# Optimization experiments

Hardware: AMD Instinct MI355X
Metric: run time of the kernel (lower is better)

## Reference

```python
import jax, jax.numpy as jnp
import numpy as np

N, E = 4096, 131072
IN_DIM, HID, OUT_DIM = 128, 64, 128
H1 = 4                       # gat1 heads
D_MODEL = HID * H1           # 256
NHEAD = 4
D_FF = 2048


def setup_inputs() -> dict:
    key = jax.random.key(0)
    ks = jax.random.split(key, 16)
    def w(k, shape, scale=0.05):
        return jax.random.normal(k, shape, dtype=jnp.float32) * scale
    return {
        "x": jax.random.normal(ks[0], (N, IN_DIM), dtype=jnp.float32),
        "edge_index": jax.random.randint(ks[1], (2, E), 0, N, dtype=jnp.int32),
        "gat1_w": w(ks[2], (H1 * HID, IN_DIM)),
        "gat1_asrc": w(ks[3], (H1, HID)),
        "gat1_adst": w(ks[4], (H1, HID)),
        "gat1_b": jnp.zeros((H1 * HID,), jnp.float32),
        "in_proj_w": w(ks[5], (3 * D_MODEL, D_MODEL)),
        "in_proj_b": jnp.zeros((3 * D_MODEL,), jnp.float32),
        "out_proj_w": w(ks[6], (D_MODEL, D_MODEL)),
        "out_proj_b": jnp.zeros((D_MODEL,), jnp.float32),
        "lin1_w": w(ks[7], (D_FF, D_MODEL)),
        "lin1_b": jnp.zeros((D_FF,), jnp.float32),
        "lin2_w": w(ks[8], (D_MODEL, D_FF)),
        "lin2_b": jnp.zeros((D_MODEL,), jnp.float32),
        "ln1_g": jnp.ones((D_MODEL,), jnp.float32),
        "ln1_b": jnp.zeros((D_MODEL,), jnp.float32),
        "ln2_g": jnp.ones((D_MODEL,), jnp.float32),
        "ln2_b": jnp.zeros((D_MODEL,), jnp.float32),
        "gat2_w": w(ks[9], (OUT_DIM, D_MODEL)),
        "gat2_asrc": w(ks[10], (1, OUT_DIM)),
        "gat2_adst": w(ks[11], (1, OUT_DIM)),
        "gat2_b": jnp.zeros((OUT_DIM,), jnp.float32),
    }


def _add_self_loops(ei, n):
    loops = jnp.arange(n, dtype=ei.dtype)
    return jnp.concatenate([ei, jnp.stack([loops, loops])], axis=1)


def _segment_softmax(logits, seg, n):
    # numerically stable softmax over edges grouped by destination node
    m = jax.ops.segment_max(logits, seg, num_segments=n)
    m = jnp.where(jnp.isfinite(m), m, 0.0)
    e = jnp.exp(logits - m[seg])
    s = jax.ops.segment_sum(e, seg, num_segments=n)
    return e / (s[seg] + 1e-16)


def _gat(x, ei, W, asrc, adst, b, heads, out_ch):
    n = x.shape[0]
    h = (x @ W.T).reshape(n, heads, out_ch)          # [N,H,C]
    al_s = jnp.einsum('nhc,hc->nh', h, asrc)
    al_d = jnp.einsum('nhc,hc->nh', h, adst)
    src, dst = ei[0], ei[1]
    logits = jax.nn.leaky_relu(al_s[src] + al_d[dst], 0.2)   # [E,H]
    alpha = _segment_softmax(logits, dst, n)
    out = jax.ops.segment_sum(h[src] * alpha[:, :, None], dst, num_segments=n)
    return out.reshape(n, heads * out_ch) + b


def _ln(x, g, b):
    mu = x.mean(-1, keepdims=True)
    v = x.var(-1, keepdims=True)
    return (x - mu) / jnp.sqrt(v + 1e-5) * g + b


def _forward(x, edge_index, gat1_w, gat1_asrc, gat1_adst, gat1_b,
             in_proj_w, in_proj_b, out_proj_w, out_proj_b,
             lin1_w, lin1_b, lin2_w, lin2_b, ln1_g, ln1_b, ln2_g, ln2_b,
             gat2_w, gat2_asrc, gat2_adst, gat2_b):
    n = x.shape[0]
    ei = _add_self_loops(edge_index, n)
    h = jax.nn.elu(_gat(x, ei, gat1_w, gat1_asrc, gat1_adst, gat1_b, H1, HID))  # [N, 256]
    # TransformerEncoderLayer (post-norm, relu, no dropout in eval)
    hd = D_MODEL // NHEAD
    qkv = h @ in_proj_w.T + in_proj_b
    q, k, v = jnp.split(qkv, 3, axis=-1)
    q = q.reshape(n, NHEAD, hd)
    k = k.reshape(n, NHEAD, hd)
    v = v.reshape(n, NHEAD, hd)
    scores = jnp.einsum('qhd,khd->hqk', q, k) / jnp.sqrt(jnp.float32(hd))
    attn = jax.nn.softmax(scores, axis=-1)
    o = jnp.einsum('hqk,khd->qhd', attn, v).reshape(n, D_MODEL)
    o = o @ out_proj_w.T + out_proj_b
    h = _ln(h + o, ln1_g, ln1_b)
    ff = jax.nn.relu(h @ lin1_w.T + lin1_b) @ lin2_w.T + lin2_b
    h = _ln(h + ff, ln2_g, ln2_b)
    return _gat(h, ei, gat2_w, gat2_asrc, gat2_adst, gat2_b, 1, OUT_DIM)


def reference(x, edge_index, gat1_w, gat1_asrc, gat1_adst, gat1_b,
              in_proj_w, in_proj_b, out_proj_w, out_proj_b,
              lin1_w, lin1_b, lin2_w, lin2_b, ln1_g, ln1_b, ln2_g, ln2_b,
              gat2_w, gat2_asrc, gat2_adst, gat2_b):
    return _forward(x, edge_index, gat1_w, gat1_asrc, gat1_adst, gat1_b,
                    in_proj_w, in_proj_b, out_proj_w, out_proj_b,
                    lin1_w, lin1_b, lin2_w, lin2_b, ln1_g, ln1_b, ln2_g, ln2_b,
                    gat2_w, gat2_asrc, gat2_adst, gat2_b)
```

## Files before the change

kernel.cpp:

```cpp
#include <hip/hip_runtime.h>
#include <hip/hip_bf16.h>
#include <math.h>

#define NN 4096
#define NE 131072
#define EE (NE + NN)

typedef unsigned short u16;
typedef short s8v __attribute__((ext_vector_type(8)));
typedef float f4v __attribute__((ext_vector_type(4)));
typedef float f16v __attribute__((ext_vector_type(16)));

__device__ inline u16 f2b(float f) {
  __hip_bfloat16 h = __float2bfloat16(f);
  return __builtin_bit_cast(u16, h);
}
__device__ inline float b2f(u16 v) {
  unsigned int u = ((unsigned int)v) << 16;
  return __builtin_bit_cast(float, u);
}

__global__ void k_count(const int* __restrict__ ei, int* __restrict__ deg) {
  int e = blockIdx.x * 256 + threadIdx.x;
  if (e >= EE) return;
  int dst = (e < NE) ? ei[NE + e] : (e - NE);
  atomicAdd(&deg[dst], 1);
}

__global__ __launch_bounds__(1024) void k_scan(const int* __restrict__ deg, int* __restrict__ rowptr) {
  __shared__ int lds[1024];
  int t = threadIdx.x;
  int v0 = deg[t*4+0], v1 = deg[t*4+1], v2 = deg[t*4+2], v3 = deg[t*4+3];
  int s1 = v0+v1, s2 = s1+v2, s3 = s2+v3;
  lds[t] = s3;
  __syncthreads();
  for (int off = 1; off < 1024; off <<= 1) {
    int add = (t >= off) ? lds[t-off] : 0;
    __syncthreads();
    lds[t] += add;
    __syncthreads();
  }
  int base = lds[t] - s3;
  rowptr[t*4+1] = base + v0;
  rowptr[t*4+2] = base + s1;
  rowptr[t*4+3] = base + s2;
  rowptr[t*4+4] = base + s3;
  if (t == 0) rowptr[0] = 0;
}

__global__ void k_scatter(const int* __restrict__ ei, const int* __restrict__ rowptr,
                          int* __restrict__ cursor, int* __restrict__ csr_src) {
  int e = blockIdx.x * 256 + threadIdx.x;
  if (e >= EE) return;
  int src, dst;
  if (e < NE) { src = ei[e]; dst = ei[NE + e]; }
  else { src = e - NE; dst = src; }
  int pos = rowptr[dst] + atomicAdd(&cursor[dst], 1);
  csr_src[pos] = src;
}

__global__ __launch_bounds__(256) void k_f2b_all(
    const float* a0, u16* b0, int e0, const float* a1, u16* b1, int e1,
    const float* a2, u16* b2, int e2, const float* a3, u16* b3, int e3,
    const float* a4, u16* b4, int e4, const float* a5, u16* b5, int e5,
    const float* a6, u16* b6, int e6)
{
  int i = blockIdx.x * 256 + threadIdx.x;
  const float* s; u16* d; int base;
  if      (i < e0) { s=a0; d=b0; base=0;  }
  else if (i < e1) { s=a1; d=b1; base=e0; }
  else if (i < e2) { s=a2; d=b2; base=e1; }
  else if (i < e3) { s=a3; d=b3; base=e2; }
  else if (i < e4) { s=a4; d=b4; base=e3; }
  else if (i < e5) { s=a5; d=b5; base=e4; }
  else if (i < e6) { s=a6; d=b6; base=e5; }
  else return;
  int j = i - base;
  float4 v = ((const float4*)s)[j];
  u16 r[4] = {f2b(v.x), f2b(v.y), f2b(v.z), f2b(v.w)};
  *(uint2*)(d + (size_t)j*4) = *(uint2*)r;
}

template<int HEADS, int C>
__global__ __launch_bounds__(256) void k_alogits(
    const u16* __restrict__ featb, const float* __restrict__ asrc,
    const float* __restrict__ adst, float* __restrict__ als, float* __restrict__ ald)
{
  constexpr int F = HEADS * C;
  int n = blockIdx.x, t = threadIdx.x;
  __shared__ float red[F];
  float f = b2f(featb[(size_t)n*F + t]);
  int hh = t / C, cc = t % C;
  red[t] = f * asrc[t];
  __syncthreads();
  for (int off = C/2; off > 0; off >>= 1) {
    float add = (cc < off) ? red[t + off] : 0.f;
    __syncthreads();
    if (cc < off) red[t] += add;
    __syncthreads();
  }
  if (cc == 0) als[(size_t)n*HEADS + hh] = red[t];
  __syncthreads();
  red[t] = f * adst[t];
  __syncthreads();
  for (int off = C/2; off > 0; off >>= 1) {
    float add = (cc < off) ? red[t + off] : 0.f;
    __syncthreads();
    if (cc < off) red[t] += add;
    __syncthreads();
  }
  if (cc == 0) ald[(size_t)n*HEADS + hh] = red[t];
}

template<int HEADS, int C, bool DO_ELU, bool WB>
__global__ __launch_bounds__(256) void k_gat_agg(
    const u16* __restrict__ featb, const float* __restrict__ als,
    const float* __restrict__ ald, const float* __restrict__ bias,
    const int* __restrict__ rowptr, const int* __restrict__ csr_src,
    float* __restrict__ out, u16* __restrict__ outb)
{
  constexpr int F = HEADS * C;
  int n = blockIdx.x, t = threadIdx.x;
  __shared__ float m_sh[HEADS], s_sh[HEADS];
  int start = rowptr[n];
  int deg = rowptr[n+1] - start;
  int lane = t & 63, wv = t >> 6;
  for (int hh = wv; hh < HEADS; hh += F/64) {
    float adl = ald[(size_t)n*HEADS + hh];
    float mx = -INFINITY;
    for (int i = lane; i < deg; i += 64) {
      int s = csr_src[start + i];
      float lg = als[(size_t)s*HEADS + hh] + adl;
      lg = (lg > 0.f) ? lg : 0.2f * lg;
      mx = fmaxf(mx, lg);
    }
    #pragma unroll
    for (int off = 32; off; off >>= 1) mx = fmaxf(mx, __shfl_xor(mx, off));
    float sm = 0.f;
    for (int i = lane; i < deg; i += 64) {
      int s = csr_src[start + i];
      float lg = als[(size_t)s*HEADS + hh] + adl;
      lg = (lg > 0.f) ? lg : 0.2f * lg;
      sm += expf(lg - mx);
    }
    #pragma unroll
    for (int off = 32; off; off >>= 1) sm += __shfl_xor(sm, off);
    if (lane == 0) { m_sh[hh] = mx; s_sh[hh] = sm; }
  }
  __syncthreads();
  int hh = t / C;
  float adl = ald[(size_t)n*HEADS + hh];
  float mh = m_sh[hh];
  float acc0 = 0.f, acc1 = 0.f;
  int i = 0;
  for (; i + 1 < deg; i += 2) {
    int s0 = csr_src[start + i];
    int s1 = csr_src[start + i + 1];
    float lg0 = als[(size_t)s0*HEADS + hh] + adl;
    float lg1 = als[(size_t)s1*HEADS + hh] + adl;
    lg0 = (lg0 > 0.f) ? lg0 : 0.2f * lg0;
    lg1 = (lg1 > 0.f) ? lg1 : 0.2f * lg1;
    float p0 = expf(lg0 - mh);
    float p1 = expf(lg1 - mh);
    acc0 += p0 * b2f(featb[(size_t)s0*F + t]);
    acc1 += p1 * b2f(featb[(size_t)s1*F + t]);
  }
  if (i < deg) {
    int s0 = csr_src[start + i];
    float lg0 = als[(size_t)s0*HEADS + hh] + adl;
    lg0 = (lg0 > 0.f) ? lg0 : 0.2f * lg0;
    acc0 += expf(lg0 - mh) * b2f(featb[(size_t)s0*F + t]);
  }
  float o = (acc0 + acc1) / (s_sh[hh] + 1e-16f) + bias[t];
  if (DO_ELU) o = (o > 0.f) ? o : (expf(o) - 1.f);
  out[(size_t)n*F + t] = o;
  if (WB) outb[(size_t)n*F + t] = f2b(o);
}

template<int MODE>
__global__ __launch_bounds__(256) void k_gemm_mfma(
    const u16* __restrict__ A, const u16* __restrict__ B,
    const float* __restrict__ bias, float* __restrict__ Cf, u16* __restrict__ Cb,
    u16* __restrict__ Qb, u16* __restrict__ Kb, u16* __restrict__ Vt,
    int M, int N, int K)
{
  __shared__ u16 Al[64*64];
  __shared__ u16 Bl[64*64];
  char* Ab = (char*)Al;
  char* Bb = (char*)Bl;
  const int t = threadIdx.x;
  const int lane = t & 63;
  const int lr = lane & 15, lk = lane >> 4;
  const int wid = t >> 6;
  const int wm = wid & 1, wn = wid >> 1;
  const int m0 = blockIdx.y * 64, n0 = blockIdx.x * 64;

  f4v acc[2][2];
  #pragma unroll
  for (int mi = 0; mi < 2; ++mi)
    #pragma unroll
    for (int ni = 0; ni < 2; ++ni)
      acc[mi][ni] = f4v{0.f, 0.f, 0.f, 0.f};

  for (int k0 = 0; k0 < K; k0 += 64) {
    #pragma unroll
    for (int i = 0; i < 2; ++i) {
      int idx = t + i*256;
      int row = idx >> 3, ch = idx & 7;
      s8v av = *(const s8v*)(A + (size_t)(m0 + row)*K + k0 + ch*8);
      *(s8v*)(Ab + row*128 + ((ch*16) ^ ((row & 7) << 4))) = av;
      s8v bv = *(const s8v*)(B + (size_t)(n0 + row)*K + k0 + ch*8);
      *(s8v*)(Bb + row*128 + ((ch*16) ^ ((row & 7) << 4))) = bv;
    }
    __syncthreads();
    #pragma unroll
    for (int ks = 0; ks < 2; ++ks) {
      s8v af[2], bfr[2];
      #pragma unroll
      for (int mi = 0; mi < 2; ++mi) {
        int row = wm*32 + mi*16 + lr;
        int ch = ks*4 + lk;
        af[mi] = *(const s8v*)(Ab + row*128 + ((ch*16) ^ ((row & 7) << 4)));
      }
      #pragma unroll
      for (int ni = 0; ni < 2; ++ni) {
        int row = wn*32 + ni*16 + lr;
        int ch = ks*4 + lk;
        bfr[ni] = *(const s8v*)(Bb + row*128 + ((ch*16) ^ ((row & 7) << 4)));
      }
      #pragma unroll
      for (int mi = 0; mi < 2; ++mi)
        #pragma unroll
        for (int ni = 0; ni < 2; ++ni)
          acc[mi][ni] = __builtin_amdgcn_mfma_f32_16x16x32_bf16(af[mi], bfr[ni], acc[mi][ni], 0, 0, 0);
    }
    __syncthreads();
  }
  #pragma unroll
  for (int ni = 0; ni < 2; ++ni) {
    int col = n0 + wn*32 + ni*16 + lr;
    float bc = bias ? bias[col] : 0.f;
    #pragma unroll
    for (int mi = 0; mi < 2; ++mi) {
      int row0 = m0 + wm*32 + mi*16 + lk*4;
      float v[4];
      #pragma unroll
      for (int r = 0; r < 4; ++r) {
        v[r] = acc[mi][ni][r] + bc;
        if (MODE == 1) v[r] = fmaxf(v[r], 0.f);
      }
      if (MODE == 0) {
        #pragma unroll
        for (int r = 0; r < 4; ++r) Cf[(size_t)(row0 + r)*N + col] = v[r];
      } else if (MODE == 1 || MODE == 2) {
        #pragma unroll
        for (int r = 0; r < 4; ++r) Cb[(size_t)(row0 + r)*N + col] = f2b(v[r]);
      } else {
        if (col < 512) {
          int head = (col >> 6) & 3;
          int d = col & 63;
          u16* dst = ((col < 256) ? Qb : Kb) + (size_t)head*262144 + d;
          #pragma unroll
          for (int r = 0; r < 4; ++r) dst[(size_t)(row0 + r)*64] = f2b(v[r]);
        } else {
          int cc = col - 512;
          int head = cc >> 6;
          int d = cc & 63;
          int quad = row0 & 12;
          int qs = (quad == 4) ? 8 : ((quad == 8) ? 4 : quad);
          size_t nphys = (size_t)((row0 & ~15) | qs);
          u16 o4[4];
          #pragma unroll
          for (int r = 0; r < 4; ++r) o4[r] = f2b(v[r]);
          *(uint2*)(Vt + (size_t)head*262144 + (size_t)d*4096 + nphys) = *(uint2*)o4;
        }
      }
    }
  }
}

__global__ __launch_bounds__(256) void k_gemm_sk(
    const u16* __restrict__ A, const u16* __restrict__ B,
    float* __restrict__ Po, int M, int N, int K)
{
  __shared__ u16 Al[64*64];
  __shared__ u16 Bl[64*64];
  char* Ab = (char*)Al;
  char* Bb = (char*)Bl;
  const int t = threadIdx.x;
  const int lane = t & 63;
  const int lr = lane & 15, lk = lane >> 4;
  const int wid = t >> 6;
  const int wm = wid & 1, wn = wid >> 1;
  const int m0 = blockIdx.y * 64, n0 = blockIdx.x * 64;
  const int z = blockIdx.z;
  const int ksl = K >> 2;

  f4v acc[2][2];
  #pragma unroll
  for (int mi = 0; mi < 2; ++mi)
    #pragma unroll
    for (int ni = 0; ni < 2; ++ni)
      acc[mi][ni] = f4v{0.f, 0.f, 0.f, 0.f};

  for (int k0 = z*ksl; k0 < (z+1)*ksl; k0 += 64) {
    #pragma unroll
    for (int i = 0; i < 2; ++i) {
      int idx = t + i*256;
      int row = idx >> 3, ch = idx & 7;
      s8v av = *(const s8v*)(A + (size_t)(m0 + row)*K + k0 + ch*8);
      *(s8v*)(Ab + row*128 + ((ch*16) ^ ((row & 7) << 4))) = av;
      s8v bv = *(const s8v*)(B + (size_t)(n0 + row)*K + k0 + ch*8);
      *(s8v*)(Bb + row*128 + ((ch*16) ^ ((row & 7) << 4))) = bv;
    }
    __syncthreads();
    #pragma unroll
    for (int ks = 0; ks < 2; ++ks) {
      s8v af[2], bfr[2];
      #pragma unroll
      for (int mi = 0; mi < 2; ++mi) {
        int row = wm*32 + mi*16 + lr;
        int ch = ks*4 + lk;
        af[mi] = *(const s8v*)(Ab + row*128 + ((ch*16) ^ ((row & 7) << 4)));
      }
      #pragma unroll
      for (int ni = 0; ni < 2; ++ni) {
        int row = wn*32 + ni*16 + lr;
        int ch = ks*4 + lk;
        bfr[ni] = *(const s8v*)(Bb + row*128 + ((ch*16) ^ ((row & 7) << 4)));
      }
      #pragma unroll
      for (int mi = 0; mi < 2; ++mi)
        #pragma unroll
        for (int ni = 0; ni < 2; ++ni)
          acc[mi][ni] = __builtin_amdgcn_mfma_f32_16x16x32_bf16(af[mi], bfr[ni], acc[mi][ni], 0, 0, 0);
    }
    __syncthreads();
  }
  float* Pz = Po + (size_t)z * M * N;
  #pragma unroll
  for (int ni = 0; ni < 2; ++ni) {
    int col = n0 + wn*32 + ni*16 + lr;
    #pragma unroll
    for (int mi = 0; mi < 2; ++mi) {
      int row0 = m0 + wm*32 + mi*16 + lk*4;
      #pragma unroll
      for (int r = 0; r < 4; ++r)
        Pz[(size_t)(row0 + r)*N + col] = acc[mi][ni][r];
    }
  }
}

template<bool WB>
__global__ __launch_bounds__(256) void k_ln(
    const float* __restrict__ a, const float* __restrict__ res,
    const float* __restrict__ g, const float* __restrict__ bb,
    float* __restrict__ out, u16* __restrict__ outb)
{
  int n = blockIdx.x, t = threadIdx.x;
  __shared__ float part[4];
  float v = a[(size_t)n*256 + t] + res[(size_t)n*256 + t];
  float s = v;
  #pragma unroll
  for (int off = 32; off; off >>= 1) s += __shfl_xor(s, off);
  if ((t & 63) == 0) part[t >> 6] = s;
  __syncthreads();
  float mean = (part[0] + part[1] + part[2] + part[3]) * (1.f/256.f);
  __syncthreads();
  float d = v - mean;
  float s2 = d * d;
  #pragma unroll
  for (int off = 32; off; off >>= 1) s2 += __shfl_xor(s2, off);
  if ((t & 63) == 0) part[t >> 6] = s2;
  __syncthreads();
  float var = (part[0] + part[1] + part[2] + part[3]) * (1.f/256.f);
  float rstd = rsqrtf(var + 1e-5f);
  float o = d * rstd * g[t] + bb[t];
  out[(size_t)n*256 + t] = o;
  if (WB) outb[(size_t)n*256 + t] = f2b(o);
}

template<bool WB>
__global__ __launch_bounds__(256) void k_ln_sk(
    const float* __restrict__ Po, const float* __restrict__ bias,
    const float* __restrict__ res, const float* __restrict__ g,
    const float* __restrict__ bb, float* __restrict__ out, u16* __restrict__ outb)
{
  int n = blockIdx.x, t = threadIdx.x;
  __shared__ float part[4];
  const size_t MN = (size_t)NN * 256;
  size_t idx = (size_t)n*256 + t;
  float v = Po[idx] + Po[MN + idx] + Po[2*MN + idx] + Po[3*MN + idx]
          + bias[t] + res[idx];
  float s = v;
  #pragma unroll
  for (int off = 32; off; off >>= 1) s += __shfl_xor(s, off);
  if ((t & 63) == 0) part[t >> 6] = s;
  __syncthreads();
  float mean = (part[0] + part[1] + part[2] + part[3]) * (1.f/256.f);
  __syncthreads();
  float d = v - mean;
  float s2 = d * d;
  #pragma unroll
  for (int off = 32; off; off >>= 1) s2 += __shfl_xor(s2, off);
  if ((t & 63) == 0) part[t >> 6] = s2;
  __syncthreads();
  float var = (part[0] + part[1] + part[2] + part[3]) * (1.f/256.f);
  float rstd = rsqrtf(var + 1e-5f);
  float o = d * rstd * g[t] + bb[t];
  out[idx] = o;
  if (WB) outb[idx] = f2b(o);
}

__global__ __launch_bounds__(512) void k_attn2(
    const u16* __restrict__ Qb, const u16* __restrict__ Kb,
    const u16* __restrict__ Vt, u16* __restrict__ attno_b)
{
  const int strip = blockIdx.x;
  const int head  = blockIdx.y;
  const int q0 = strip * 32;
  const int t = threadIdx.x;
  const int s = t >> 6;
  const int l = t & 63;
  const int lq = l & 31;
  const int lh = l >> 5;

  __shared__ float lds_O[4][32][68];
  __shared__ float lds_m[4][32];
  __shared__ float lds_l[4][32];

  const u16* Qh = Qb + (size_t)head * (4096*64);
  const u16* Kh = Kb + (size_t)head * (4096*64);
  const u16* Vh = Vt + (size_t)head * (64*4096);

  s8v qf[4];
#pragma unroll
  for (int dc = 0; dc < 4; ++dc)
    qf[dc] = *(const s8v*)(Qh + (size_t)(q0 + lq)*64 + dc*16 + lh*8);

  f16v accO[2];
#pragma unroll
  for (int dm = 0; dm < 2; ++dm)
#pragma unroll
    for (int i = 0; i < 16; ++i) accO[dm][i] = 0.f;

  float mrow = -INFINITY, lrow = 0.f;
  const float CE = 0.18033688011112042f;

  const int kt0 = s * 512;
  for (int kt = kt0; kt < kt0 + 512; kt += 64) {
    f16v st[2];
#pragma unroll
    for (int c = 0; c < 2; ++c)
#pragma unroll
      for (int i = 0; i < 16; ++i) st[c][i] = 0.f;
    __builtin_amdgcn_s_setprio(1);
#pragma unroll
    for (int dc = 0; dc < 4; ++dc) {
      s8v kf0 = *(const s8v*)(Kh + (size_t)(kt + lq)*64 + dc*16 + lh*8);
      s8v kf1 = *(const s8v*)(Kh + (size_t)(kt + 32 + lq)*64 + dc*16 + lh*8);
      st[0] = __builtin_amdgcn_mfma_f32_32x32x16_bf16(kf0, qf[dc], st[0], 0, 0, 0);
      st[1] = __builtin_amdgcn_mfma_f32_32x32x16_bf16(kf1, qf[dc], st[1], 0, 0, 0);
    }
    __builtin_amdgcn_s_setprio(0);
    float tm[16];
#pragma unroll
    for (int i = 0; i < 8; ++i) tm[i]   = fmaxf(st[0][2*i], st[0][2*i+1]);
#pragma unroll
    for (int i = 0; i < 8; ++i) tm[8+i] = fmaxf(st[1][2*i], st[1][2*i+1]);
#pragma unroll
    for (int w = 8; w >= 1; w >>= 1)
#pragma unroll
      for (int i = 0; i < 8; ++i) if (i < w) tm[i] = fmaxf(tm[i], tm[i+w]);
    float mx = fmaxf(tm[0], __shfl_xor(tm[0], 32));
    float mn;
    if (__all(mx - mrow <= 66.0f)) {
      mn = mrow;
    } else {
      mn = fmaxf(mrow, mx);
      float sc = exp2f((mrow - mn) * CE);
      mrow = mn;
      lrow *= sc;
#pragma unroll
      for (int dm = 0; dm < 2; ++dm)
#pragma unroll
        for (int i = 0; i < 16; ++i) accO[dm][i] *= sc;
    }
    float ts[16];
#pragma unroll
    for (int c = 0; c < 2; ++c)
#pragma unroll
      for (int i = 0; i < 16; ++i)
        st[c][i] = exp2f((st[c][i] - mn) * CE);
#pragma unroll
    for (int i = 0; i < 8; ++i) ts[i]   = st[0][2*i] + st[0][2*i+1];
#pragma unroll
    for (int i = 0; i < 8; ++i) ts[8+i] = st[1][2*i] + st[1][2*i+1];
#pragma unroll
    for (int w = 8; w >= 1; w >>= 1)
#pragma unroll
      for (int i = 0; i < 8; ++i) if (i < w) ts[i] += ts[i+w];
    float ps = ts[0] + __shfl_xor(ts[0], 32);
    lrow += ps;

#pragma unroll
    for (int c = 0; c < 2; ++c) {
#pragma unroll
      for (int kc = 0; kc < 2; ++kc) {
        union { s8v v; unsigned int w[4]; } pb;
#pragma unroll
        for (int wd = 0; wd < 4; ++wd) {
          u16 lo16 = f2b(st[c][kc*8 + wd*2]);
          u16 hi16 = f2b(st[c][kc*8 + wd*2 + 1]);
          pb.w[wd] = (unsigned int)lo16 | ((unsigned int)hi16 << 16);
        }
        __builtin_amdgcn_s_setprio(1);
#pragma unroll
        for (int dm = 0; dm < 2; ++dm) {
          s8v vf = *(const s8v*)(Vh + (size_t)(dm*32 + lq)*4096 + kt + c*32 + kc*16 + lh*8);
          accO[dm] = __builtin_amdgcn_mfma_f32_32x32x16_bf16(vf, pb.v, accO[dm], 0, 0, 0);
        }
        __builtin_amdgcn_s_setprio(0);
      }
    }
  }

#pragma unroll
  for (int lev = 0; lev < 3; ++lev) {
    const int step = 1 << lev;
    __syncthreads();
    if ((s & (2*step - 1)) == step) {
      int slot = (s - step) >> (lev + 1);
      if (l < 32) { lds_m[slot][lq] = mrow; lds_l[slot][lq] = lrow; }
#pragma unroll
      for (int dm = 0; dm < 2; ++dm)
#pragma unroll
        for (int g = 0; g < 4; ++g) {
          f4v v;
#pragma unroll
          for (int rr = 0; rr < 4; ++rr) v[rr] = accO[dm][g*4 + rr];
          *(f4v*)&lds_O[slot][lq][dm*32 + lh*4 + g*8] = v;
        }
    }
    __syncthreads();
    if ((s & (2*step - 1)) == 0) {
      int slot = s >> (lev + 1);
      float mp = lds_m[slot][lq], lp = lds_l[slot][lq];
      float M = fmaxf(mrow, mp);
      float w0 = exp2f((mrow - M) * CE);
      float w1 = exp2f((mp - M) * CE);
      lrow = lrow * w0 + lp * w1;
      mrow = M;
#pragma unroll
      for (int dm = 0; dm < 2; ++dm)
#pragma unroll
        for (int g = 0; g < 4; ++g) {
          f4v vp = *(const f4v*)&lds_O[slot][lq][dm*32 + lh*4 + g*8];
#pragma unroll
          for (int rr = 0; rr < 4; ++rr)
            accO[dm][g*4 + rr] = accO[dm][g*4 + rr] * w0 + vp[rr] * w1;
        }
    }
  }

  if (s == 0) {
    float inv = 1.f / lrow;
#pragma unroll
    for (int dm = 0; dm < 2; ++dm)
#pragma unroll
      for (int g = 0; g < 4; ++g) {
        u16 o4[4];
#pragma unroll
        for (int rr = 0; rr < 4; ++rr) o4[rr] = f2b(accO[dm][g*4 + rr] * inv);
        *(uint2*)(attno_b + (size_t)(q0 + lq)*256 + head*64 + dm*32 + lh*4 + g*8) = *(uint2*)o4;
      }
  }
}

extern "C" void kernel_launch(void* const* d_in, const int* in_sizes, int n_in,
                              void* d_out, int out_size, void* d_ws, size_t ws_size,
                              hipStream_t stream)
{
  const float* x       = (const float*)d_in[0];
  const int*   ei      = (const int*)d_in[1];
  const float* gat1_w  = (const float*)d_in[2];
  const float* gat1_as = (const float*)d_in[3];
  const float* gat1_ad = (const float*)d_in[4];
  const float* gat1_b  = (const float*)d_in[5];
  const float* inp_w   = (const float*)d_in[6];
  const float* inp_b   = (const float*)d_in[7];
  const float* outp_w  = (const float*)d_in[8];
  const float* outp_b  = (const float*)d_in[9];
  const float* lin1_w  = (const float*)d_in[10];
  const float* lin1_b  = (const float*)d_in[11];
  const float* lin2_w  = (const float*)d_in[12];
  const float* lin2_b  = (const float*)d_in[13];
  const float* ln1_g   = (const float*)d_in[14];
  const float* ln1_bb  = (const float*)d_in[15];
  const float* ln2_g   = (const float*)d_in[16];
  const float* ln2_bb  = (const float*)d_in[17];
  const float* gat2_w  = (const float*)d_in[18];
  const float* gat2_as = (const float*)d_in[19];
  const float* gat2_ad = (const float*)d_in[20];
  const float* gat2_b  = (const float*)d_in[21];
  float* out = (float*)d_out;
  (void)in_sizes; (void)n_in; (void)out_size; (void)ws_size;

  char* ws = (char*)d_ws;
  size_t off = 0;
  auto nxt = [&](size_t bytes) { size_t r = off; off += (bytes + 255) & ~(size_t)255; return r; };
  int* deg      = (int*)(ws + nxt((size_t)NN*4));
  int* cursor   = (int*)(ws + nxt((size_t)NN*4));
  int* rowptr   = (int*)(ws + nxt((size_t)(NN+1)*4));
  int* csr_src  = (int*)(ws + nxt((size_t)EE*4));
  float* al1s   = (float*)(ws + nxt((size_t)NN*4*4));
  float* al1d   = (float*)(ws + nxt((size_t)NN*4*4));
  float* hgat1  = (float*)(ws + nxt((size_t)NN*256*4));
  float* tmp256 = (float*)(ws + nxt((size_t)NN*256*4));
  float* hln1   = (float*)(ws + nxt((size_t)NN*256*4));
  float* hln2   = (float*)(ws + nxt((size_t)NN*256*4));
  float* Po     = (float*)(ws + nxt((size_t)4*NN*256*4));
  float* al2s   = (float*)(ws + nxt((size_t)NN*4));
  float* al2d   = (float*)(ws + nxt((size_t)NN*4));
  u16* x_b      = (u16*)(ws + nxt((size_t)NN*128*2));
  u16* feat1_b  = (u16*)(ws + nxt((size_t)NN*256*2));
  u16* feat2_b  = (u16*)(ws + nxt((size_t)NN*128*2));
  u16* hgat1_b  = (u16*)(ws + nxt((size_t)NN*256*2));
  u16* attno_b  = (u16*)(ws + nxt((size_t)NN*256*2));
  u16* hln1_b   = (u16*)(ws + nxt((size_t)NN*256*2));
  u16* hln2_b   = (u16*)(ws + nxt((size_t)NN*256*2));
  u16* ff1_b    = (u16*)(ws + nxt((size_t)NN*2048*2));
  u16* Qb       = (u16*)(ws + nxt((size_t)4*4096*64*2));
  u16* Kb       = (u16*)(ws + nxt((size_t)4*4096*64*2));
  u16* Vt       = (u16*)(ws + nxt((size_t)4*4096*64*2));
  u16* inp_w_b  = (u16*)(ws + nxt((size_t)768*256*2));
  u16* outp_w_b = (u16*)(ws + nxt((size_t)256*256*2));
  u16* lin1_w_b = (u16*)(ws + nxt((size_t)2048*256*2));
  u16* lin2_w_b = (u16*)(ws + nxt((size_t)256*2048*2));
  u16* gat1_w_b = (u16*)(ws + nxt((size_t)256*128*2));
  u16* gat2_w_b = (u16*)(ws + nxt((size_t)128*256*2));

  hipMemsetAsync(deg, 0, (size_t)NN*4, stream);
  hipMemsetAsync(cursor, 0, (size_t)NN*4, stream);
  k_count<<<(EE+255)/256, 256, 0, stream>>>(ei, deg);
  k_scan<<<1, 1024, 0, stream>>>(deg, rowptr);
  k_scatter<<<(EE+255)/256, 256, 0, stream>>>(ei, rowptr, cursor, csr_src);

  k_f2b_all<<<1856, 256, 0, stream>>>(
      inp_w,  inp_w_b,  49152,
      outp_w, outp_w_b, 65536,
      lin1_w, lin1_w_b, 196608,
      lin2_w, lin2_w_b, 327680,
      gat1_w, gat1_w_b, 335872,
      gat2_w, gat2_w_b, 344064,
      x,      x_b,      475136);

  k_gemm_mfma<2><<<dim3(4, 64), 256, 0, stream>>>(x_b, gat1_w_b, nullptr, nullptr, feat1_b, nullptr, nullptr, nullptr, NN, 256, 128);
  k_alogits<4,64><<<NN, 256, 0, stream>>>(feat1_b, gat1_as, gat1_ad, al1s, al1d);
  k_gat_agg<4,64,true,true><<<NN, 256, 0, stream>>>(feat1_b, al1s, al1d, gat1_b, rowptr, csr_src, hgat1, hgat1_b);

  k_gemm_mfma<3><<<dim3(12, 64), 256, 0, stream>>>(hgat1_b, inp_w_b, inp_b, nullptr, nullptr, Qb, Kb, Vt, NN, 768, 256);
  k_attn2<<<dim3(128, 4), 512, 0, stream>>>(Qb, Kb, Vt, attno_b);
  k_gemm_mfma<0><<<dim3(4, 64), 256, 0, stream>>>(attno_b, outp_w_b, outp_b, tmp256, nullptr, nullptr, nullptr, nullptr, NN, 256, 256);
  k_ln<true><<<NN, 256, 0, stream>>>(tmp256, hgat1, ln1_g, ln1_bb, hln1, hln1_b);
  k_gemm_mfma<1><<<dim3(32, 64), 256, 0, stream>>>(hln1_b, lin1_w_b, lin1_b, nullptr, ff1_b, nullptr, nullptr, nullptr, NN, 2048, 256);
  k_gemm_sk<<<dim3(4, 64, 4), 256, 0, stream>>>(ff1_b, lin2_w_b, Po, NN, 256, 2048);
  k_ln_sk<true><<<NN, 256, 0, stream>>>(Po, lin2_b, hln1, ln2_g, ln2_bb, hln2, hln2_b);

  k_gemm_mfma<2><<<dim3(2, 64), 256, 0, stream>>>(hln2_b, gat2_w_b, nullptr, nullptr, feat2_b, nullptr, nullptr, nullptr, NN, 128, 256);
  k_alogits<1,128><<<NN, 128, 0, stream>>>(feat2_b, gat2_as, gat2_ad, al2s, al2d);
  k_gat_agg<1,128,false,false><<<NN, 128, 0, stream>>>(feat2_b, al2s, al2d, gat2_b, rowptr, csr_src, out, nullptr);
}
```

Baseline: 307.6 us.

## Split attention over keys, retile FFN GEMMs, cache GAT alphas, shuffle reductions

```diff
diff --git a/kernel.cpp b/kernel.cpp
--- a/kernel.cpp
+++ b/kernel.cpp
@@ -88,28 +88,29 @@
 {
   constexpr int F = HEADS * C;
   int n = blockIdx.x, t = threadIdx.x;
-  __shared__ float red[F];
   float f = b2f(featb[(size_t)n*F + t]);
-  int hh = t / C, cc = t % C;
-  red[t] = f * asrc[t];
-  __syncthreads();
-  for (int off = C/2; off > 0; off >>= 1) {
-    float add = (cc < off) ? red[t + off] : 0.f;
-    __syncthreads();
-    if (cc < off) red[t] += add;
-    __syncthreads();
-  }
-  if (cc == 0) als[(size_t)n*HEADS + hh] = red[t];
-  __syncthreads();
-  red[t] = f * adst[t];
-  __syncthreads();
-  for (int off = C/2; off > 0; off >>= 1) {
-    float add = (cc < off) ? red[t + off] : 0.f;
-    __syncthreads();
-    if (cc < off) red[t] += add;
-    __syncthreads();
-  }
-  if (cc == 0) ald[(size_t)n*HEADS + hh] = red[t];
+  float ps = f * asrc[t];
+  float pd = f * adst[t];
+  #pragma unroll
+  for (int off = 32; off; off >>= 1) {
+    ps += __shfl_xor(ps, off);
+    pd += __shfl_xor(pd, off);
+  }
+  if constexpr (C == 64) {
+    if ((t & 63) == 0) {
+      int hh = t >> 6;
+      als[(size_t)n*HEADS + hh] = ps;
+      ald[(size_t)n*HEADS + hh] = pd;
+    }
+  } else {
+    __shared__ float sh[2][2];
+    if ((t & 63) == 0) { sh[t>>6][0] = ps; sh[t>>6][1] = pd; }
+    __syncthreads();
+    if (t == 0) {
+      als[n] = sh[0][0] + sh[1][0];
+      ald[n] = sh[0][1] + sh[1][1];
+    }
+  }
 }
 
 template<int HEADS, int C, bool DO_ELU, bool WB>
@@ -122,6 +123,8 @@
   constexpr int F = HEADS * C;
   int n = blockIdx.x, t = threadIdx.x;
   __shared__ float m_sh[HEADS], s_sh[HEADS];
+  __shared__ float alpha_sh[HEADS][64];
+  __shared__ int src_sh[64];
   int start = rowptr[n];
   int deg = rowptr[n+1] - start;
   int lane = t & 63, wv = t >> 6;
@@ -149,27 +152,29 @@
   }
   __syncthreads();
   int hh = t / C;
-  float adl = ald[(size_t)n*HEADS + hh];
-  float mh = m_sh[hh];
+  int hh2 = t >> 6;
+  int ia = t & 63;
   float acc0 = 0.f, acc1 = 0.f;
-  int i = 0;
-  for (; i + 1 < deg; i += 2) {
-    int s0 = csr_src[start + i];
-    int s1 = csr_src[start + i + 1];
-    float lg0 = als[(size_t)s0*HEADS + hh] + adl;
-    float lg1 = als[(size_t)s1*HEADS + hh] + adl;
-    lg0 = (lg0 > 0.f) ? lg0 : 0.2f * lg0;
-    lg1 = (lg1 > 0.f) ? lg1 : 0.2f * lg1;
-    float p0 = expf(lg0 - mh);
-    float p1 = expf(lg1 - mh);
-    acc0 += p0 * b2f(featb[(size_t)s0*F + t]);
-    acc1 += p1 * b2f(featb[(size_t)s1*F + t]);
-  }
-  if (i < deg) {
-    int s0 = csr_src[start + i];
-    float lg0 = als[(size_t)s0*HEADS + hh] + adl;
-    lg0 = (lg0 > 0.f) ? lg0 : 0.2f * lg0;
-    acc0 += expf(lg0 - mh) * b2f(featb[(size_t)s0*F + t]);
+  for (int c0 = 0; c0 < deg; c0 += 64) {
+    int cn = min(64, deg - c0);
+    if (hh2 < HEADS && ia < cn) {
+      int s = csr_src[start + c0 + ia];
+      if (hh2 == 0) src_sh[ia] = s;
+      float lg = als[(size_t)s*HEADS + hh2] + ald[(size_t)n*HEADS + hh2];
+      lg = (lg > 0.f) ? lg : 0.2f * lg;
+      alpha_sh[hh2][ia] = expf(lg - m_sh[hh2]);
+    }
+    __syncthreads();
+    int i = 0;
+    for (; i + 1 < cn; i += 2) {
+      int s0 = src_sh[i], s1 = src_sh[i+1];
+      float a0 = alpha_sh[hh][i], a1 = alpha_sh[hh][i+1];
+      acc0 += a0 * b2f(featb[(size_t)s0*F + t]);
+      acc1 += a1 * b2f(featb[(size_t)s1*F + t]);
+    }
+    if (i < cn)
+      acc0 += alpha_sh[hh][i] * b2f(featb[(size_t)src_sh[i]*F + t]);
+    __syncthreads();
   }
   float o = (acc0 + acc1) / (s_sh[hh] + 1e-16f) + bias[t];
   if (DO_ELU) o = (o > 0.f) ? o : (expf(o) - 1.f);
@@ -245,14 +250,11 @@
       int row0 = m0 + wm*32 + mi*16 + lk*4;
       float v[4];
       #pragma unroll
-      for (int r = 0; r < 4; ++r) {
-        v[r] = acc[mi][ni][r] + bc;
-        if (MODE == 1) v[r] = fmaxf(v[r], 0.f);
-      }
+      for (int r = 0; r < 4; ++r) v[r] = acc[mi][ni][r] + bc;
       if (MODE == 0) {
         #pragma unroll
         for (int r = 0; r < 4; ++r) Cf[(size_t)(row0 + r)*N + col] = v[r];
-      } else if (MODE == 1 || MODE == 2) {
+      } else if (MODE == 2) {
         #pragma unroll
         for (int r = 0; r < 4; ++r) Cb[(size_t)(row0 + r)*N + col] = f2b(v[r]);
       } else {
@@ -279,74 +281,87 @@
   }
 }
 
-__global__ __launch_bounds__(256) void k_gemm_sk(
+template<int MODE>
+__global__ __launch_bounds__(256) void k_gemm2(
     const u16* __restrict__ A, const u16* __restrict__ B,
-    float* __restrict__ Po, int M, int N, int K)
-{
-  __shared__ u16 Al[64*64];
+    const float* __restrict__ bias, float* __restrict__ Cf, u16* __restrict__ Cb,
+    int M, int N, int K, int ksl)
+{
+  __shared__ u16 Al[128*64];
   __shared__ u16 Bl[64*64];
   char* Ab = (char*)Al;
   char* Bb = (char*)Bl;
   const int t = threadIdx.x;
   const int lane = t & 63;
   const int lr = lane & 15, lk = lane >> 4;
-  const int wid = t >> 6;
-  const int wm = wid & 1, wn = wid >> 1;
-  const int m0 = blockIdx.y * 64, n0 = blockIdx.x * 64;
+  const int wv = t >> 6;
+  const int m0 = blockIdx.y * 128, n0 = blockIdx.x * 64;
   const int z = blockIdx.z;
-  const int ksl = K >> 2;
-
-  f4v acc[2][2];
+  const int kbeg = z * ksl, kend = kbeg + ksl;
+
+  f4v acc[2][4];
   #pragma unroll
   for (int mi = 0; mi < 2; ++mi)
     #pragma unroll
-    for (int ni = 0; ni < 2; ++ni)
+    for (int ni = 0; ni < 4; ++ni)
       acc[mi][ni] = f4v{0.f, 0.f, 0.f, 0.f};
 
-  for (int k0 = z*ksl; k0 < (z+1)*ksl; k0 += 64) {
-    #pragma unroll
-    for (int i = 0; i < 2; ++i) {
+  for (int k0 = kbeg; k0 < kend; k0 += 64) {
+    #pragma unroll
+    for (int i = 0; i < 4; ++i) {
       int idx = t + i*256;
       int row = idx >> 3, ch = idx & 7;
       s8v av = *(const s8v*)(A + (size_t)(m0 + row)*K + k0 + ch*8);
       *(s8v*)(Ab + row*128 + ((ch*16) ^ ((row & 7) << 4))) = av;
+    }
+    #pragma unroll
+    for (int i = 0; i < 2; ++i) {
+      int idx = t + i*256;
+      int row = idx >> 3, ch = idx & 7;
       s8v bv = *(const s8v*)(B + (size_t)(n0 + row)*K + k0 + ch*8);
       *(s8v*)(Bb + row*128 + ((ch*16) ^ ((row & 7) << 4))) = bv;
     }
     __syncthreads();
     #pragma unroll
     for (int ks = 0; ks < 2; ++ks) {
-      s8v af[2], bfr[2];
+      s8v af[2], bfr[4];
       #pragma unroll
       for (int mi = 0; mi < 2; ++mi) {
-        int row = wm*32 + mi*16 + lr;
+        int row = wv*32 + mi*16 + lr;
         int ch = ks*4 + lk;
         af[mi] = *(const s8v*)(Ab + row*128 + ((ch*16) ^ ((row & 7) << 4)));
       }
       #pragma unroll
-      for (int ni = 0; ni < 2; ++ni) {
-        int row = wn*32 + ni*16 + lr;
+      for (int ni = 0; ni < 4; ++ni) {
+        int row = ni*16 + lr;
         int ch = ks*4 + lk;
         bfr[ni] = *(const s8v*)(Bb + row*128 + ((ch*16) ^ ((row & 7) << 4)));
       }
       #pragma unroll
       for (int mi = 0; mi < 2; ++mi)
         #pragma unroll
-        for (int ni = 0; ni < 2; ++ni)
+        for (int ni = 0; ni < 4; ++ni)
           acc[mi][ni] = __builtin_amdgcn_mfma_f32_16x16x32_bf16(af[mi], bfr[ni], acc[mi][ni], 0, 0, 0);
     }
     __syncthreads();
   }
-  float* Pz = Po + (size_t)z * M * N;
-  #pragma unroll
-  for (int ni = 0; ni < 2; ++ni) {
-    int col = n0 + wn*32 + ni*16 + lr;
+  #pragma unroll
+  for (int ni = 0; ni < 4; ++ni) {
+    int col = n0 + ni*16 + lr;
+    float bc = (MODE == 4) ? 0.f : bias[col];
     #pragma unroll
     for (int mi = 0; mi < 2; ++mi) {
-      int row0 = m0 + wm*32 + mi*16 + lk*4;
+      int row0 = m0 + wv*32 + mi*16 + lk*4;
       #pragma unroll
-      for (int r = 0; r < 4; ++r)
-        Pz[(size_t)(row0 + r)*N + col] = acc[mi][ni][r];
+      for (int r = 0; r < 4; ++r) {
+        float v = acc[mi][ni][r] + bc;
+        if (MODE == 1) {
+          v = fmaxf(v, 0.f);
+          Cb[(size_t)(row0 + r)*N + col] = f2b(v);
+        } else {
+          (Cf + (size_t)z*M*N)[(size_t)(row0 + r)*N + col] = v;
+        }
+      }
     }
   }
 }
@@ -414,10 +429,12 @@
 
 __global__ __launch_bounds__(512) void k_attn2(
     const u16* __restrict__ Qb, const u16* __restrict__ Kb,
-    const u16* __restrict__ Vt, u16* __restrict__ attno_b)
+    const u16* __restrict__ Vt, float* __restrict__ op,
+    float* __restrict__ mb, float* __restrict__ lb)
 {
   const int strip = blockIdx.x;
   const int head  = blockIdx.y;
+  const int z     = blockIdx.z;
   const int q0 = strip * 32;
   const int t = threadIdx.x;
   const int s = t >> 6;
@@ -447,14 +464,13 @@
   float mrow = -INFINITY, lrow = 0.f;
   const float CE = 0.18033688011112042f;
 
-  const int kt0 = s * 512;
-  for (int kt = kt0; kt < kt0 + 512; kt += 64) {
+  const int kt0 = z * 2048 + s * 256;
+  for (int kt = kt0; kt < kt0 + 256; kt += 64) {
     f16v st[2];
 #pragma unroll
     for (int c = 0; c < 2; ++c)
 #pragma unroll
       for (int i = 0; i < 16; ++i) st[c][i] = 0.f;
-    __builtin_amdgcn_s_setprio(1);
 #pragma unroll
     for (int dc = 0; dc < 4; ++dc) {
       s8v kf0 = *(const s8v*)(Kh + (size_t)(kt + lq)*64 + dc*16 + lh*8);
@@ -462,46 +478,30 @@
       st[0] = __builtin_amdgcn_mfma_f32_32x32x16_bf16(kf0, qf[dc], st[0], 0, 0, 0);
       st[1] = __builtin_amdgcn_mfma_f32_32x32x16_bf16(kf1, qf[dc], st[1], 0, 0, 0);
     }
-    __builtin_amdgcn_s_setprio(0);
-    float tm[16];
-#pragma unroll
-    for (int i = 0; i < 8; ++i) tm[i]   = fmaxf(st[0][2*i], st[0][2*i+1]);
-#pragma unroll
-    for (int i = 0; i < 8; ++i) tm[8+i] = fmaxf(st[1][2*i], st[1][2*i+1]);
-#pragma unroll
-    for (int w = 8; w >= 1; w >>= 1)
-#pragma unroll
-      for (int i = 0; i < 8; ++i) if (i < w) tm[i] = fmaxf(tm[i], tm[i+w]);
-    float mx = fmaxf(tm[0], __shfl_xor(tm[0], 32));
-    float mn;
-    if (__all(mx - mrow <= 66.0f)) {
-      mn = mrow;
-    } else {
-      mn = fmaxf(mrow, mx);
-      float sc = exp2f((mrow - mn) * CE);
-      mrow = mn;
-      lrow *= sc;
-#pragma unroll
-      for (int dm = 0; dm < 2; ++dm)
-#pragma unroll
-        for (int i = 0; i < 16; ++i) accO[dm][i] *= sc;
-    }
-    float ts[16];
+    float mx = st[0][0];
+#pragma unroll
+    for (int i = 1; i < 16; ++i) mx = fmaxf(mx, st[0][i]);
+#pragma unroll
+    for (int i = 0; i < 16; ++i) mx = fmaxf(mx, st[1][i]);
+    mx = fmaxf(mx, __shfl_xor(mx, 32));
+    float mn = fmaxf(mrow, mx);
+    float sc = exp2f((mrow - mn) * CE);
+    mrow = mn;
+    float ps = 0.f;
 #pragma unroll
     for (int c = 0; c < 2; ++c)
 #pragma unroll
-      for (int i = 0; i < 16; ++i)
-        st[c][i] = exp2f((st[c][i] - mn) * CE);
-#pragma unroll
-    for (int i = 0; i < 8; ++i) ts[i]   = st[0][2*i] + st[0][2*i+1];
-#pragma unroll
-    for (int i = 0; i < 8; ++i) ts[8+i] = st[1][2*i] + st[1][2*i+1];
-#pragma unroll
-    for (int w = 8; w >= 1; w >>= 1)
-#pragma unroll
-      for (int i = 0; i < 8; ++i) if (i < w) ts[i] += ts[i+w];
-    float ps = ts[0] + __shfl_xor(ts[0], 32);
-    lrow += ps;
+      for (int i = 0; i < 16; ++i) {
+        float p = exp2f((st[c][i] - mn) * CE);
+        st[c][i] = p;
+        ps += p;
+      }
+    ps += __shfl_xor(ps, 32);
+    lrow = lrow * sc + ps;
+#pragma unroll
+    for (int dm = 0; dm < 2; ++dm)
+#pragma unroll
+      for (int i = 0; i < 16; ++i) accO[dm][i] *= sc;
 
 #pragma unroll
     for (int c = 0; c < 2; ++c) {
@@ -514,13 +514,11 @@
           u16 hi16 = f2b(st[c][kc*8 + wd*2 + 1]);
           pb.w[wd] = (unsigned int)lo16 | ((unsigned int)hi16 << 16);
         }
-        __builtin_amdgcn_s_setprio(1);
 #pragma unroll
         for (int dm = 0; dm < 2; ++dm) {
           s8v vf = *(const s8v*)(Vh + (size_t)(dm*32 + lq)*4096 + kt + c*32 + kc*16 + lh*8);
           accO[dm] = __builtin_amdgcn_mfma_f32_32x32x16_bf16(vf, pb.v, accO[dm], 0, 0, 0);
         }
-        __builtin_amdgcn_s_setprio(0);
       }
     }
   }
@@ -564,17 +562,45 @@
   }
 
   if (s == 0) {
-    float inv = 1.f / lrow;
+    int pb = (z*4 + head)*128 + strip;
+    if (l < 32) { mb[pb*32 + lq] = mrow; lb[pb*32 + lq] = lrow; }
 #pragma unroll
     for (int dm = 0; dm < 2; ++dm)
 #pragma unroll
       for (int g = 0; g < 4; ++g) {
-        u16 o4[4];
-#pragma unroll
-        for (int rr = 0; rr < 4; ++rr) o4[rr] = f2b(accO[dm][g*4 + rr] * inv);
-        *(uint2*)(attno_b + (size_t)(q0 + lq)*256 + head*64 + dm*32 + lh*4 + g*8) = *(uint2*)o4;
-      }
-  }
+        f4v v;
+#pragma unroll
+        for (int rr = 0; rr < 4; ++rr) v[rr] = accO[dm][g*4 + rr];
+        *(f4v*)&op[(size_t)pb*2048 + lq*64 + dm*32 + lh*4 + g*8] = v;
+      }
+  }
+}
+
+__global__ __launch_bounds__(256) void k_attn_mrg(
+    const float* __restrict__ op, const float* __restrict__ mb,
+    const float* __restrict__ lb, u16* __restrict__ attno_b)
+{
+  const int strip = blockIdx.x;
+  const int head = blockIdx.y;
+  const int t = threadIdx.x;
+  const int q = t >> 3;
+  const int d0 = (t & 7) * 8;
+  const float CE = 0.18033688011112042f;
+  int p0 = (0*4 + head)*128 + strip;
+  int p1 = (1*4 + head)*128 + strip;
+  float m0 = mb[p0*32 + q], m1 = mb[p1*32 + q];
+  float M = fmaxf(m0, m1);
+  float w0 = exp2f((m0 - M) * CE);
+  float w1 = exp2f((m1 - M) * CE);
+  float L = w0 * lb[p0*32 + q] + w1 * lb[p1*32 + q];
+  float inv = 1.f / L;
+  const float* o0 = op + (size_t)p0*2048 + q*64 + d0;
+  const float* o1 = op + (size_t)p1*2048 + q*64 + d0;
+  u16 o8[8];
+#pragma unroll
+  for (int i = 0; i < 8; ++i)
+    o8[i] = f2b((w0 * o0[i] + w1 * o1[i]) * inv);
+  *(uint4*)(attno_b + (size_t)(strip*32 + q)*256 + head*64 + d0) = *(uint4*)o8;
 }
 
 extern "C" void kernel_launch(void* const* d_in, const int* in_sizes, int n_in,
@@ -640,6 +666,10 @@
   u16* gat1_w_b = (u16*)(ws + nxt((size_t)256*128*2));
   u16* gat2_w_b = (u16*)(ws + nxt((size_t)128*256*2));
 
+  float* a_op = Po;
+  float* a_mb = Po + (size_t)1024*2048;
+  float* a_lb = a_mb + 32768;
+
   hipMemsetAsync(deg, 0, (size_t)NN*4, stream);
   hipMemsetAsync(cursor, 0, (size_t)NN*4, stream);
   k_count<<<(EE+255)/256, 256, 0, stream>>>(ei, deg);
@@ -660,11 +690,12 @@
   k_gat_agg<4,64,true,true><<<NN, 256, 0, stream>>>(feat1_b, al1s, al1d, gat1_b, rowptr, csr_src, hgat1, hgat1_b);
 
   k_gemm_mfma<3><<<dim3(12, 64), 256, 0, stream>>>(hgat1_b, inp_w_b, inp_b, nullptr, nullptr, Qb, Kb, Vt, NN, 768, 256);
-  k_attn2<<<dim3(128, 4), 512, 0, stream>>>(Qb, Kb, Vt, attno_b);
+  k_attn2<<<dim3(128, 4, 2), 512, 0, stream>>>(Qb, Kb, Vt, a_op, a_mb, a_lb);
+  k_attn_mrg<<<dim3(128, 4), 256, 0, stream>>>(a_op, a_mb, a_lb, attno_b);
   k_gemm_mfma<0><<<dim3(4, 64), 256, 0, stream>>>(attno_b, outp_w_b, outp_b, tmp256, nullptr, nullptr, nullptr, nullptr, NN, 256, 256);
   k_ln<true><<<NN, 256, 0, stream>>>(tmp256, hgat1, ln1_g, ln1_bb, hln1, hln1_b);
-  k_gemm_mfma<1><<<dim3(32, 64), 256, 0, stream>>>(hln1_b, lin1_w_b, lin1_b, nullptr, ff1_b, nullptr, nullptr, nullptr, NN, 2048, 256);
-  k_gemm_sk<<<dim3(4, 64, 4), 256, 0, stream>>>(ff1_b, lin2_w_b, Po, NN, 256, 2048);
+  k_gemm2<1><<<dim3(32, 32), 256, 0, stream>>>(hln1_b, lin1_w_b, lin1_b, nullptr, ff1_b, NN, 2048, 256, 256);
+  k_gemm2<4><<<dim3(4, 32, 4), 256, 0, stream>>>(ff1_b, lin2_w_b, nullptr, Po, nullptr, NN, 256, 2048, 512);
   k_ln_sk<true><<<NN, 256, 0, stream>>>(Po, lin2_b, hln1, ln2_g, ln2_bb, hln2, hln2_b);
 
   k_gemm_mfma<2><<<dim3(2, 64), 256, 0, stream>>>(hln2_b, gat2_w_b, nullptr, nullptr, feat2_b, nullptr, nullptr, nullptr, NN, 128, 256);
```

New measurement: 300.1 us. 2.4% less time.
